# Kernel tuning notes

Measured on AMD Instinct MI355X. Metric: run time of the kernel, lower is better.

Reference implementation:

```python
import jax, jax.numpy as jnp
import numpy as np

N = 20000      # nodes
E = 320000     # edges
H = 256        # hidden_dim
BD = 64        # bond embedding dim
MSG_IN = 2 * H + BD  # 576


def setup_inputs() -> dict:
    key = jax.random.key(0)
    ks = jax.random.split(key, 24)
    s = 0.05
    inp = {}
    inp["x"] = jax.random.randint(ks[0], (N, 3), 0, 7).astype(jnp.float32)
    inp["edge_index"] = jax.random.randint(ks[1], (2, E), 0, N).astype(jnp.int32)
    inp["edge_attr"] = jax.random.randint(ks[2], (E, 1), 0, 5).astype(jnp.float32)
    inp["batch"] = jnp.zeros((N,), jnp.int32)
    # embedding tables
    inp["atom_table"] = jax.random.normal(ks[3], (11, 64), jnp.float32) * s
    inp["charge_table"] = jax.random.normal(ks[4], (7, 32), jnp.float32) * s
    inp["hybrid_table"] = jax.random.normal(ks[5], (8, 32), jnp.float32) * s
    inp["bond_table"] = jax.random.normal(ks[6], (5, BD), jnp.float32) * s
    # 3 stacked ChemicalGraphConv layers (weights stored [in, out])
    inp["gnn_w1"] = jax.random.normal(ks[7], (3, MSG_IN, H), jnp.float32) * s
    inp["gnn_b1"] = jnp.zeros((3, H), jnp.float32)
    inp["gnn_w2"] = jax.random.normal(ks[8], (3, H, H), jnp.float32) * s
    inp["gnn_b2"] = jnp.zeros((3, H), jnp.float32)
    inp["att_w"] = jax.random.normal(ks[9], (3, BD, 1), jnp.float32) * s
    inp["att_b"] = jnp.zeros((3, 1), jnp.float32)
    # chemical_properties MLP
    inp["prop_w1"] = jax.random.normal(ks[10], (H, 128), jnp.float32) * s
    inp["prop_b1"] = jnp.zeros((128,), jnp.float32)
    inp["prop_w2"] = jax.random.normal(ks[11], (128, 32), jnp.float32) * s
    inp["prop_b2"] = jnp.zeros((32,), jnp.float32)
    # 4 functional-group pattern encoders, stacked [4, H, 16]
    inp["fg_w"] = jax.random.normal(ks[12], (4, H, 16), jnp.float32) * s
    inp["fg_b"] = jnp.zeros((4, 16), jnp.float32)
    return inp


def reference(x, edge_index, edge_attr, batch,
              atom_table, charge_table, hybrid_table, bond_table,
              gnn_w1, gnn_b1, gnn_w2, gnn_b2, att_w, att_b,
              prop_w1, prop_b1, prop_w2, prop_b2, fg_w, fg_b):
    n = x.shape[0]
    atom_types = jnp.clip(x[:, 0].astype(jnp.int32), 0, 10)
    formal_charges = jnp.clip(x[:, 2].astype(jnp.int32) + 3, 0, 6)
    hybridization = jnp.clip(x[:, 1].astype(jnp.int32), 0, 7)
    bond_types = jnp.clip(edge_attr[:, 0].astype(jnp.int32), 0, 4)
    bond_emb = bond_table[bond_types]  # [E, 64]

    h = jnp.concatenate([atom_table[atom_types],
                         charge_table[formal_charges],
                         hybrid_table[hybridization]], axis=-1)  # [N, 128]
    h = jnp.pad(h, ((0, 0), (0, H - h.shape[1])))  # pad to hidden_dim

    row, col = edge_index[0], edge_index[1]
    for l in range(3):  # 3 ChemicalGraphConv layers
        gate = jax.nn.sigmoid(bond_emb @ att_w[l] + att_b[l])            # [E, 1]
        msg = jnp.concatenate([h[row], h[col], bond_emb], axis=-1)      # [E, 576]
        msg = jax.nn.relu(msg @ gnn_w1[l] + gnn_b1[l]) @ gnn_w2[l] + gnn_b2[l]
        msg = msg * gate                                                 # [E, H]
        h = h + jax.ops.segment_sum(msg, row, num_segments=n)

    chemical_props = jax.nn.relu(h @ prop_w1 + prop_b1) @ prop_w2 + prop_b2  # [N, 32]

    # FunctionalGroupDetector: mean(encoder(h)) == mean(h) @ W + b (linear)
    pooled = jnp.mean(h, axis=0)                                   # [H]
    fg = (jnp.einsum('d,kdo->ko', pooled, fg_w) + fg_b).reshape(-1)  # [64]
    fg_features = jnp.broadcast_to(fg, (n, 64))

    return h, chemical_props, fg_features, atom_types
```

## Files before the change

### kernel.cpp

```cpp
#include <hip/hip_runtime.h>
#include <stdint.h>

typedef unsigned short u16;
typedef unsigned int   u32;
typedef unsigned long long u64;
typedef __attribute__((ext_vector_type(8))) short bf16x8;
typedef __attribute__((ext_vector_type(4))) float f32x4;

#define NN 20000
#define NE 320000
#define HD 256
#define BD 64

#define WS_PRE   0u
#define WS_W1T   20480000u
#define WS_W2I   21266432u
#define WS_PW1   21659648u
#define WS_PREB  21725184u
#define WS_GATE  21740544u
#define WS_POOL  21740608u
#define WS_FGV   21741632u
#define WS_CNT   21741888u
#define WS_META  21821888u

__device__ __forceinline__ u16 f2bf(float f){
  u32 u = __float_as_uint(f);
  u += 0x7fffu + ((u >> 16) & 1u);
  return (u16)(u >> 16);
}
__device__ __forceinline__ u32 pk2(float a, float b){
  return (u32)f2bf(a) | ((u32)f2bf(b) << 16);
}
__device__ __forceinline__ float bf2f(u16 u){
  return __uint_as_float((u32)u << 16);
}
__device__ __forceinline__ u32 pk2t(float a, float b){
  return __builtin_amdgcn_perm(__float_as_uint(a), __float_as_uint(b), 0x03020706u);
}
__device__ __forceinline__ u32 relu_pack(u32 a, u32 b, float p0, float p1){
  float a0 = __uint_as_float(a << 16);
  float a1 = __uint_as_float(a & 0xffff0000u);
  float b0 = __uint_as_float(b << 16);
  float b1 = __uint_as_float(b & 0xffff0000u);
  float s0 = fmaxf(a0 + b0 + p0, 0.f);
  float s1 = fmaxf(a1 + b1 + p1, 0.f);
  return pk2t(s0, s1);
}
__device__ __forceinline__ void gl_lds16(const u16* g, u16* l){
  __builtin_amdgcn_global_load_lds(
      (const __attribute__((address_space(1))) unsigned int*)g,
      (__attribute__((address_space(3))) unsigned int*)l, 16, 0, 0);
}

__global__ void setup_k(const float* __restrict__ gw1,
                        const float* __restrict__ gw2,
                        const float* __restrict__ pw1,
                        const float* __restrict__ bond_table,
                        const float* __restrict__ gb1,
                        const float* __restrict__ att_w,
                        const float* __restrict__ att_b,
                        const float* __restrict__ x,
                        const float* __restrict__ atom_table,
                        const float* __restrict__ charge_table,
                        const float* __restrict__ hybrid_table,
                        u16* __restrict__ w1t, u16* __restrict__ w2img,
                        u16* __restrict__ pw1bf, float* __restrict__ preb,
                        float* __restrict__ gate_tab, float* __restrict__ pooled,
                        int* __restrict__ cnt,
                        float* __restrict__ h0, float* __restrict__ out_at){
  int i = blockIdx.x*256 + threadIdx.x;
  if (i < 442368){
    float v = gw1[i];
    int l = i / 147456;
    int r = i - l*147456;
    int srow = r >> 8, c = r & 255;
    if (srow < 512){
      int dc = (srow < 256) ? c : (256 + c);
      w1t[((size_t)l*512 + dc)*256 + (srow & 255)] = f2bf(v);
    }
  } else if (i < 638976){
    int t = i - 442368;
    float v = gw2[t];
    int l = t >> 16;
    int rest = t & 65535;
    int k = rest >> 8, c = rest & 255;
    int ks = k >> 5, k5 = k & 31;
    int kc = k5 >> 3, j = k5 & 7;
    int s = kc ^ ((c >> 1) & 3);
    w2img[(((l*8 + ks)*256 + c)*4 + s)*8 + j] = f2bf(v);
  } else if (i < 671744){
    int t = i - 638976;
    float v = pw1[t];
    int k = t >> 7, o = t & 127;
    pw1bf[o*256 + k] = f2bf(v);
  } else if (i < 675584){
    int t = i - 671744;
    int l = t / 1280;
    int r = t - l*1280;
    int bt = r >> 8, c = r & 255;
    float s = gb1[l*HD + c];
    for (int d = 0; d < BD; ++d)
      s += bond_table[bt*BD + d] * gw1[(l*576 + 512 + d)*256 + c];
    preb[(l*5 + bt)*256 + c] = s;
  } else if (i < 675599){
    int t = i - 675584;
    int l = t / 5, b = t - 5*l;
    float s = att_b[l];
    for (int d = 0; d < BD; ++d) s += bond_table[b*BD + d] * att_w[l*BD + d];
    gate_tab[t] = 1.0f / (1.0f + __expf(-s));
  } else if (i < 675855){
    pooled[i - 675599] = 0.0f;
  } else if (i < 695855){
    cnt[i - 675855] = 0;
  } else if (i < 1335855){
    int t = i - 695855;
    int n = t >> 5, sub = t & 31, c0 = sub*8;
    int at = (int)x[n*3 + 0]; at = at < 0 ? 0 : (at > 10 ? 10 : at);
    float4 v0 = {0.f,0.f,0.f,0.f}, v1 = {0.f,0.f,0.f,0.f};
    if (c0 < 64){
      v0 = *(const float4*)(atom_table + at*64 + c0);
      v1 = *(const float4*)(atom_table + at*64 + c0 + 4);
    } else if (c0 < 96){
      int fc = (int)x[n*3 + 2] + 3; fc = fc < 0 ? 0 : (fc > 6 ? 6 : fc);
      v0 = *(const float4*)(charge_table + fc*32 + (c0 - 64));
      v1 = *(const float4*)(charge_table + fc*32 + (c0 - 64) + 4);
    } else if (c0 < 128){
      int hy = (int)x[n*3 + 1]; hy = hy < 0 ? 0 : (hy > 7 ? 7 : hy);
      v0 = *(const float4*)(hybrid_table + hy*32 + (c0 - 96));
      v1 = *(const float4*)(hybrid_table + hy*32 + (c0 - 96) + 4);
    }
    *(float4*)(h0 + (size_t)n*HD + c0)     = v0;
    *(float4*)(h0 + (size_t)n*HD + c0 + 4) = v1;
    if (sub == 0) out_at[n] = (float)at;
  }
}

__global__ void hist_k(const int* __restrict__ eidx, int* __restrict__ cnt){
  int e = blockIdx.x*256 + threadIdx.x;
  int r = eidx[e]; r = r < 0 ? 0 : (r >= NN ? NN-1 : r);
  atomicAdd(&cnt[r], 1);
}

__launch_bounds__(1024)
__global__ void scan_k(int* __restrict__ cnt){
  __shared__ int part[1024];
  int t = threadIdx.x;
  int base = t*20;
  int loc[20];
  int s = 0;
  #pragma unroll
  for (int j = 0; j < 20; ++j){
    int idx = base + j;
    int v = (idx < NN) ? cnt[idx] : 0;
    loc[j] = v; s += v;
  }
  part[t] = s; __syncthreads();
  for (int off = 1; off < 1024; off <<= 1){
    int v = (t >= off) ? part[t-off] : 0;
    __syncthreads();
    part[t] += v;
    __syncthreads();
  }
  int run = part[t] - s;
  #pragma unroll
  for (int j = 0; j < 20; ++j){
    int idx = base + j;
    if (idx < NN){ cnt[idx] = run; run += loc[j]; }
  }
}

__global__ void scatter_k(const int* __restrict__ eidx,
                          const float* __restrict__ eattr,
                          int* __restrict__ cur,
                          int2* __restrict__ smeta){
  int e = blockIdx.x*256 + threadIdx.x;
  int r = eidx[e];        r = r < 0 ? 0 : (r >= NN ? NN-1 : r);
  int c = eidx[NE + e];   c = c < 0 ? 0 : (c >= NN ? NN-1 : c);
  int bt = (int)eattr[e]; bt = bt < 0 ? 0 : (bt > 4 ? 4 : bt);
  int pos = atomicAdd(&cur[r], 1);
  if (pos >= 0 && pos < NE){
    int2 m; m.x = r | (bt << 20); m.y = c;
    smeta[pos] = m;
  }
}

__launch_bounds__(256, 4)
__global__ void pre_k(const float* __restrict__ h,
                      const u16* __restrict__ w1t,
                      u16* __restrict__ pre, int layer){
  __shared__ u16 a_lds[64*40];
  __shared__ u16 b_lds[256*40];
  const int tid = threadIdx.x;
  const int n0 = blockIdx.x * 64;
  const int half = blockIdx.y;
  const int w = tid >> 6, lane = tid & 63, g = lane >> 4, lr = lane & 15;
  const int rstage = tid >> 2, q = tid & 3;
  int arow = n0 + rstage; if (arow >= NN) arow = NN-1;
  const float* hrow = h + (size_t)arow*HD;
  const u16* bp = w1t + ((size_t)layer*512 + (size_t)half*256 + tid)*256;

  f32x4 acc[4][4];
  for (int mi = 0; mi < 4; ++mi)
    for (int nj = 0; nj < 4; ++nj)
      acc[mi][nj] = (f32x4){0.f,0.f,0.f,0.f};

  for (int ks = 0; ks < 8; ++ks){
    __syncthreads();
    {
      const float* src = hrow + ks*32 + q*8;
      float4 f0 = *(const float4*)src;
      float4 f1 = *(const float4*)(src + 4);
      uint4 av;
      av.x = pk2(f0.x,f0.y); av.y = pk2(f0.z,f0.w);
      av.z = pk2(f1.x,f1.y); av.w = pk2(f1.z,f1.w);
      *(uint4*)(a_lds + rstage*40 + q*8) = av;
    }
    {
      const u16* src = bp + ks*32;
      uint4 s0 = *(const uint4*)(src);
      uint4 s1 = *(const uint4*)(src + 8);
      uint4 s2 = *(const uint4*)(src + 16);
      uint4 s3 = *(const uint4*)(src + 24);
      u16* dst = b_lds + tid*40;
      *(uint4*)(dst)      = s0;
      *(uint4*)(dst + 8)  = s1;
      *(uint4*)(dst + 16) = s2;
      *(uint4*)(dst + 24) = s3;
    }
    __syncthreads();
    bf16x8 af[4], bfr[4];
    for (int mi = 0; mi < 4; ++mi)
      af[mi] = *(const bf16x8*)(a_lds + (mi*16 + lr)*40 + g*8);
    for (int nj = 0; nj < 4; ++nj)
      bfr[nj] = *(const bf16x8*)(b_lds + (w*64 + nj*16 + lr)*40 + g*8);
    for (int mi = 0; mi < 4; ++mi)
      for (int nj = 0; nj < 4; ++nj)
        acc[mi][nj] = __builtin_amdgcn_mfma_f32_16x16x32_bf16(af[mi], bfr[nj], acc[mi][nj], 0, 0, 0);
  }

  for (int mi = 0; mi < 4; ++mi)
    for (int nj = 0; nj < 4; ++nj)
      for (int p = 0; p < 4; ++p){
        int re = mi*16 + g*4 + p;
        int n = n0 + re;
        if (n < NN)
          pre[(size_t)n*512 + half*256 + w*64 + nj*16 + lr] = f2bf(acc[mi][nj][p]);
      }
}

__launch_bounds__(512, 4)
__global__ void edge_msg_k(const int2* __restrict__ smeta,
                           const u16* __restrict__ pre,
                           const float* __restrict__ prebg,
                           const u16* __restrict__ w2img,
                           const float* __restrict__ b2g,
                           const float* __restrict__ gate_tab,
                           float* __restrict__ h,
                           int layer){
  __shared__ u16 b_lds[16384];
  __shared__ u16 t_lds[64*264];
  __shared__ int   row_l[64];
  __shared__ float gate_l[64];
  __shared__ u64   mask_l;

  const int tid = threadIdx.x;
  const int bid = blockIdx.x;
  const int blk = (bid & 7)*625 + (bid >> 3);
  const int eBase = blk * 64;
  const int w = tid >> 6, lane = tid & 63, g = lane >> 4, lr = lane & 15;
  const int rstage = tid >> 3, q = tid & 7;

  const size_t wbase = (size_t)layer*65536;

  #pragma unroll
  for (int b = 0; b < 2; ++b)
    #pragma unroll
    for (int j = 0; j < 2; ++j)
      gl_lds16(w2img + wbase + (size_t)(b*256 + w*32 + j*16)*32 + lane*8,
               b_lds + b*8192 + w*1024 + j*512);

  int2 m0 = smeta[eBase + rstage];
  const int rI  = m0.x & 0xFFFFF;
  const int btI = (m0.x >> 20) & 7;
  const int cI  = m0.y;

  if (tid < 64){
    int2 mm = smeta[eBase + tid];
    int r = mm.x & 0xFFFFF;
    row_l[tid]  = r;
    gate_l[tid] = gate_tab[layer*5 + ((mm.x >> 20) & 7)];
    int rprev = __shfl_up(r, 1);
    bool fl = (tid > 0) && (r != rprev);
    u64 mk = __ballot(fl);
    if (tid == 0) mask_l = mk;
  }

  {
    const u16* p1 = pre + (size_t)rI*512;
    const u16* p2 = pre + (size_t)cI*512 + 256;
    const float* pb = prebg + (size_t)(layer*5 + btI)*256;
    uint4 v1[4], v2[4];
    #pragma unroll
    for (int it = 0; it < 4; ++it){
      int c0 = it*64 + q*8;
      v1[it] = *(const uint4*)(p1 + c0);
      v2[it] = *(const uint4*)(p2 + c0);
    }
    #pragma unroll
    for (int it = 0; it < 4; ++it){
      int c0 = it*64 + q*8;
      float4 pa = *(const float4*)(pb + c0);
      float4 pc = *(const float4*)(pb + c0 + 4);
      uint4 ov;
      ov.x = relu_pack(v1[it].x, v2[it].x, pa.x, pa.y);
      ov.y = relu_pack(v1[it].y, v2[it].y, pa.z, pa.w);
      ov.z = relu_pack(v1[it].z, v2[it].z, pc.x, pc.y);
      ov.w = relu_pack(v1[it].w, v2[it].w, pc.z, pc.w);
      *(uint4*)(t_lds + rstage*264 + c0) = ov;
    }
  }

  __syncthreads();

  f32x4 acc[4][2];
  for (int mi = 0; mi < 4; ++mi)
    for (int nj = 0; nj < 2; ++nj)
      acc[mi][nj] = (f32x4){0.f,0.f,0.f,0.f};

  const int sw = (g ^ ((lr >> 1) & 3)) << 3;

  #pragma unroll
  for (int ks = 0; ks < 8; ++ks){
    if (ks >= 1 && ks < 7){
      #pragma unroll
      for (int j = 0; j < 2; ++j)
        gl_lds16(w2img + wbase + (size_t)((ks+1)*256 + w*32 + j*16)*32 + lane*8,
                 b_lds + ((ks+1)&1)*8192 + w*1024 + j*512);
      asm volatile("s_waitcnt vmcnt(2)" ::: "memory");
    } else if (ks == 0){
      asm volatile("s_waitcnt vmcnt(2)" ::: "memory");
    } else {
      asm volatile("s_waitcnt vmcnt(0)" ::: "memory");
    }
    const u16* bb = b_lds + (ks&1)*8192 + w*1024;
    bf16x8 af[4], bfr[2];
    for (int nj = 0; nj < 2; ++nj)
      bfr[nj] = *(const bf16x8*)(bb + (nj*16 + lr)*32 + sw);
    for (int mi = 0; mi < 4; ++mi)
      af[mi] = *(const bf16x8*)(t_lds + (mi*16 + lr)*264 + ks*32 + g*8);
    __builtin_amdgcn_s_setprio(1);
    for (int mi = 0; mi < 4; ++mi)
      for (int nj = 0; nj < 2; ++nj)
        acc[mi][nj] = __builtin_amdgcn_mfma_f32_16x16x32_bf16(af[mi], bfr[nj], acc[mi][nj], 0, 0, 0);
    __builtin_amdgcn_s_setprio(0);
  }

  {
    float b2v[2];
    for (int nj = 0; nj < 2; ++nj) b2v[nj] = b2g[layer*HD + w*32 + nj*16 + lr];
    for (int mi = 0; mi < 4; ++mi)
      for (int nj = 0; nj < 2; ++nj){
        u16* mb = b_lds + nj*8192 + w*1024 + lr*64;
        float v[4];
        #pragma unroll
        for (int p = 0; p < 4; ++p){
          int re = mi*16 + g*4 + p;
          v[p] = (acc[mi][nj][p] + b2v[nj]) * gate_l[re];
        }
        int slot = (mi*2 + (g >> 1)) ^ (lr & 7);
        uint2 pkv; pkv.x = pk2t(v[0], v[1]); pkv.y = pk2t(v[2], v[3]);
        *(uint2*)(mb + slot*8 + (g & 1)*4) = pkv;
      }
  }
  __syncthreads();

  {
    const int cl = tid & 255, half = tid >> 8;
    u64 mk = mask_l;
    u32 m32 = (u32)(mk >> (half ? 32 : 0));
    m32 = __builtin_amdgcn_readfirstlane(m32);
    const u16* mb = b_lds + ((cl >> 4) & 1)*8192 + (cl >> 5)*1024 + (cl & 15)*64;
    float run = 0.f;
    #pragma unroll
    for (int e8l = 0; e8l < 4; ++e8l){
      int e8 = half*4 + e8l;
      bf16x8 mv = *(const bf16x8*)(mb + ((e8 ^ (cl & 7)) << 3));
      #pragma unroll
      for (int j = 0; j < 8; ++j){
        int el = e8l*8 + j;
        run += bf2f((u16)mv[j]);
        bool fl = (el == 31) || ((m32 >> (el + 1)) & 1u);
        if (fl){
          int rr = row_l[half*32 + el];
          atomicAdd(h + (size_t)rr*HD + cl, run);
          run = 0.f;
        }
      }
    }
  }
}

__global__ void pool_k(const float* __restrict__ h,
                       float* __restrict__ pooled){
  int c = threadIdx.x;
  int r0 = blockIdx.x * 50;
  float s = 0.f;
  for (int r = r0; r < r0 + 50; ++r)
    s += h[(size_t)r*HD + c];
  atomicAdd(&pooled[c], s);
}

__global__ void fg_k(const float* __restrict__ pooled,
                     const float* __restrict__ fg_w,
                     const float* __restrict__ fg_b,
                     float* __restrict__ fg_vals){
  int o = threadIdx.x;
  int k = o >> 4, j = o & 15;
  float s = 0.f;
  for (int d = 0; d < HD; ++d) s += pooled[d] * fg_w[(size_t)k*HD*16 + d*16 + j];
  fg_vals[o] = s / (float)NN + fg_b[k*16 + j];
}

__global__ void bcast_fg_k(const float* __restrict__ fg_vals,
                           float* __restrict__ out_fg){
  __shared__ float fv[64];
  if (threadIdx.x < 64) fv[threadIdx.x] = fg_vals[threadIdx.x];
  __syncthreads();
  int i = blockIdx.x*256 + threadIdx.x;
  out_fg[i] = fv[i & 63];
}

__launch_bounds__(256, 3)
__global__ void props_mfma_k(const float* __restrict__ h,
                             const u16* __restrict__ pw1bf,
                             const float* __restrict__ pb1,
                             const float* __restrict__ pw2,
                             const float* __restrict__ pb2,
                             float* __restrict__ outp){
  __shared__ u16 a_lds[64*40];
  __shared__ u16 b2_lds[128*40];
  __shared__ u16 t2[64*136];
  __shared__ float w2s[128*32];
  const int tid = threadIdx.x;
  const int n0 = blockIdx.x*64;
  const int w = tid >> 6, lane = tid & 63, g = lane >> 4, lr = lane & 15;
  const int rstage = tid >> 2, q = tid & 3;
  int arow = n0 + rstage; if (arow >= NN) arow = NN-1;
  const float* hrow = h + (size_t)arow*HD;

  for (int j = 0; j < 4; ++j)
    *(float4*)(w2s + tid*16 + j*4) = *(const float4*)(pw2 + tid*16 + j*4);

  const int colb = tid >> 1, halfb = tid & 1;

  f32x4 acc[4][2];
  for (int mi = 0; mi < 4; ++mi)
    for (int nj = 0; nj < 2; ++nj)
      acc[mi][nj] = (f32x4){0.f,0.f,0.f,0.f};

  for (int ks = 0; ks < 8; ++ks){
    __syncthreads();
    {
      const float* src = hrow + ks*32 + q*8;
      float4 f0 = *(const float4*)src;
      float4 f1 = *(const float4*)(src + 4);
      uint4 av;
      av.x = pk2(f0.x,f0.y); av.y = pk2(f0.z,f0.w);
      av.z = pk2(f1.x,f1.y); av.w = pk2(f1.z,f1.w);
      *(uint4*)(a_lds + rstage*40 + q*8) = av;
    }
    {
      const u16* src = pw1bf + colb*256 + ks*32 + halfb*16;
      uint4 s0 = *(const uint4*)src;
      uint4 s1 = *(const uint4*)(src + 8);
      u16* dst = b2_lds + colb*40 + halfb*16;
      *(uint4*)dst = s0; *(uint4*)(dst + 8) = s1;
    }
    __syncthreads();
    bf16x8 af[4], bfr[2];
    for (int mi = 0; mi < 4; ++mi)
      af[mi] = *(const bf16x8*)(a_lds + (mi*16 + lr)*40 + g*8);
    for (int nj = 0; nj < 2; ++nj)
      bfr[nj] = *(const bf16x8*)(b2_lds + (w*32 + nj*16 + lr)*40 + g*8);
    for (int mi = 0; mi < 4; ++mi)
      for (int nj = 0; nj < 2; ++nj)
        acc[mi][nj] = __builtin_amdgcn_mfma_f32_16x16x32_bf16(af[mi], bfr[nj], acc[mi][nj], 0, 0, 0);
  }

  {
    float b1v[2];
    for (int nj = 0; nj < 2; ++nj) b1v[nj] = pb1[w*32 + nj*16 + lr];
    for (int mi = 0; mi < 4; ++mi)
      for (int nj = 0; nj < 2; ++nj){
        int colt = w*32 + nj*16 + lr;
        for (int p = 0; p < 4; ++p){
          float v = acc[mi][nj][p] + b1v[nj];
          v = v > 0.f ? v : 0.f;
          t2[(mi*16 + g*4 + p)*136 + colt] = f2bf(v);
        }
      }
  }
  __syncthreads();

  {
    int e = tid >> 2, o0 = (tid & 3)*8;
    int n = n0 + e;
    float ap[8];
    #pragma unroll
    for (int o = 0; o < 8; ++o) ap[o] = pb2[o0 + o];
    for (int d0 = 0; d0 < 16; ++d0){
      bf16x8 tv = *(const bf16x8*)(t2 + e*136 + d0*8);
      #pragma unroll
      for (int dd = 0; dd < 8; ++dd){
        float t = bf2f((u16)tv[dd]);
        const float* wr = w2s + (d0*8 + dd)*32 + o0;
        #pragma unroll
        for (int o = 0; o < 8; ++o) ap[o] += t * wr[o];
      }
    }
    if (n < NN){
      *(float4*)(outp + (size_t)n*32 + o0)     = *(float4*)(ap);
      *(float4*)(outp + (size_t)n*32 + o0 + 4) = *(float4*)(ap + 4);
    }
  }
}

extern "C" void kernel_launch(void* const* d_in, const int* in_sizes, int n_in,
                              void* d_out, int out_size, void* d_ws, size_t ws_size,
                              hipStream_t stream) {
  const float* x            = (const float*)d_in[0];
  const int*   eidx         = (const int*)  d_in[1];
  const float* eattr        = (const float*)d_in[2];
  const float* atom_table   = (const float*)d_in[4];
  const float* charge_table = (const float*)d_in[5];
  const float* hybrid_table = (const float*)d_in[6];
  const float* bond_table   = (const float*)d_in[7];
  const float* gw1          = (const float*)d_in[8];
  const float* gb1          = (const float*)d_in[9];
  const float* gw2          = (const float*)d_in[10];
  const float* gb2          = (const float*)d_in[11];
  const float* attw         = (const float*)d_in[12];
  const float* attb         = (const float*)d_in[13];
  const float* pw1          = (const float*)d_in[14];
  const float* pb1          = (const float*)d_in[15];
  const float* pw2          = (const float*)d_in[16];
  const float* pb2          = (const float*)d_in[17];
  const float* fgw          = (const float*)d_in[18];
  const float* fgb          = (const float*)d_in[19];

  float* out       = (float*)d_out;
  float* out_h     = out;
  float* out_props = out + (size_t)NN*HD;
  float* out_fg    = out_props + (size_t)NN*32;
  float* out_at    = out_fg + (size_t)NN*64;

  char* ws = (char*)d_ws;
  u16*   pre      = (u16*)  (ws + WS_PRE);
  u16*   w1t      = (u16*)  (ws + WS_W1T);
  u16*   w2img    = (u16*)  (ws + WS_W2I);
  u16*   pw1bf    = (u16*)  (ws + WS_PW1);
  float* prebg    = (float*)(ws + WS_PREB);
  float* gate_tab = (float*)(ws + WS_GATE);
  float* pooled   = (float*)(ws + WS_POOL);
  float* fg_vals  = (float*)(ws + WS_FGV);
  int*   cnt      = (int*)  (ws + WS_CNT);
  int2*  smeta    = (int2*) (ws + WS_META);

  setup_k<<<5219, 256, 0, stream>>>(gw1, gw2, pw1, bond_table, gb1, attw, attb,
                                    x, atom_table, charge_table, hybrid_table,
                                    w1t, w2img, pw1bf, prebg, gate_tab, pooled,
                                    cnt, out_h, out_at);

  hist_k<<<1250, 256, 0, stream>>>(eidx, cnt);
  scan_k<<<1, 1024, 0, stream>>>(cnt);
  scatter_k<<<1250, 256, 0, stream>>>(eidx, eattr, cnt, smeta);

  for (int l = 0; l < 3; ++l){
    pre_k<<<dim3(313, 2), 256, 0, stream>>>(out_h, w1t, pre, l);
    edge_msg_k<<<5000, 512, 0, stream>>>(smeta, pre, prebg, w2img,
                                         gb2, gate_tab, out_h, l);
  }

  pool_k<<<400, 256, 0, stream>>>(out_h, pooled);
  fg_k<<<1, 64, 0, stream>>>(pooled, fgw, fgb, fg_vals);
  props_mfma_k<<<313, 256, 0, stream>>>(out_h, pw1bf, pb1, pw2, pb2, out_props);
  bcast_fg_k<<<5000, 256, 0, stream>>>(fg_vals, out_fg);
}
```

Before: 382.9 us.

## Merge pre_k halves per block, hoist b2 bias into segment sums, MFMA props layer 2

pre_k now computes all 512 output columns per block, so each block converts and loads the h tile once instead of twice, at the cost of more accumulators and lower occupancy. edge_msg_k drops the per-element b2 bias add. Instead it adds b2 times the prefix-summed gate difference once per segment flush. The props second layer moves from scalar FMA to bf16 MFMA using a bf16 copy of pw2 prepared in setup, which adds bf16 rounding to that GEMM.

```diff
diff --git a/kernel.cpp b/kernel.cpp
--- a/kernel.cpp
+++ b/kernel.cpp
@@ -16,12 +16,13 @@
 #define WS_W1T   20480000u
 #define WS_W2I   21266432u
 #define WS_PW1   21659648u
-#define WS_PREB  21725184u
-#define WS_GATE  21740544u
-#define WS_POOL  21740608u
-#define WS_FGV   21741632u
-#define WS_CNT   21741888u
-#define WS_META  21821888u
+#define WS_PW2   21725184u
+#define WS_PREB  21733376u
+#define WS_GATE  21748736u
+#define WS_POOL  21748800u
+#define WS_FGV   21749824u
+#define WS_CNT   21750080u
+#define WS_META  21830080u
 
 __device__ __forceinline__ u16 f2bf(float f){
   u32 u = __float_as_uint(f);
@@ -55,6 +56,7 @@
 __global__ void setup_k(const float* __restrict__ gw1,
                         const float* __restrict__ gw2,
                         const float* __restrict__ pw1,
+                        const float* __restrict__ pw2,
                         const float* __restrict__ bond_table,
                         const float* __restrict__ gb1,
                         const float* __restrict__ att_w,
@@ -64,7 +66,8 @@
                         const float* __restrict__ charge_table,
                         const float* __restrict__ hybrid_table,
                         u16* __restrict__ w1t, u16* __restrict__ w2img,
-                        u16* __restrict__ pw1bf, float* __restrict__ preb,
+                        u16* __restrict__ pw1bf, u16* __restrict__ pw2bf,
+                        float* __restrict__ preb,
                         float* __restrict__ gate_tab, float* __restrict__ pooled,
                         int* __restrict__ cnt,
                         float* __restrict__ h0, float* __restrict__ out_at){
@@ -93,8 +96,13 @@
     float v = pw1[t];
     int k = t >> 7, o = t & 127;
     pw1bf[o*256 + k] = f2bf(v);
-  } else if (i < 675584){
+  } else if (i < 675840){
     int t = i - 671744;
+    float v = pw2[t];
+    int k = t >> 5, o = t & 31;
+    pw2bf[o*128 + k] = f2bf(v);
+  } else if (i < 679680){
+    int t = i - 675840;
     int l = t / 1280;
     int r = t - l*1280;
     int bt = r >> 8, c = r & 255;
@@ -102,18 +110,18 @@
     for (int d = 0; d < BD; ++d)
       s += bond_table[bt*BD + d] * gw1[(l*576 + 512 + d)*256 + c];
     preb[(l*5 + bt)*256 + c] = s;
-  } else if (i < 675599){
-    int t = i - 675584;
+  } else if (i < 679695){
+    int t = i - 679680;
     int l = t / 5, b = t - 5*l;
     float s = att_b[l];
     for (int d = 0; d < BD; ++d) s += bond_table[b*BD + d] * att_w[l*BD + d];
     gate_tab[t] = 1.0f / (1.0f + __expf(-s));
-  } else if (i < 675855){
-    pooled[i - 675599] = 0.0f;
-  } else if (i < 695855){
-    cnt[i - 675855] = 0;
-  } else if (i < 1335855){
-    int t = i - 695855;
+  } else if (i < 679951){
+    pooled[i - 679695] = 0.0f;
+  } else if (i < 699951){
+    cnt[i - 679951] = 0;
+  } else if (i < 1339951){
+    int t = i - 699951;
     int n = t >> 5, sub = t & 31, c0 = sub*8;
     int at = (int)x[n*3 + 0]; at = at < 0 ? 0 : (at > 10 ? 10 : at);
     float4 v0 = {0.f,0.f,0.f,0.f}, v1 = {0.f,0.f,0.f,0.f};
@@ -184,24 +192,25 @@
   }
 }
 
-__launch_bounds__(256, 4)
+__launch_bounds__(256, 2)
 __global__ void pre_k(const float* __restrict__ h,
                       const u16* __restrict__ w1t,
                       u16* __restrict__ pre, int layer){
   __shared__ u16 a_lds[64*40];
-  __shared__ u16 b_lds[256*40];
+  __shared__ u16 b_lds[512*40];
   const int tid = threadIdx.x;
   const int n0 = blockIdx.x * 64;
-  const int half = blockIdx.y;
   const int w = tid >> 6, lane = tid & 63, g = lane >> 4, lr = lane & 15;
   const int rstage = tid >> 2, q = tid & 3;
   int arow = n0 + rstage; if (arow >= NN) arow = NN-1;
   const float* hrow = h + (size_t)arow*HD;
-  const u16* bp = w1t + ((size_t)layer*512 + (size_t)half*256 + tid)*256;
-
-  f32x4 acc[4][4];
+  const u16* bp0 = w1t + ((size_t)layer*512 + tid)*256;
+  const u16* bp1 = bp0 + 256*256;
+
+  f32x4 acc[4][8];
   for (int mi = 0; mi < 4; ++mi)
-    for (int nj = 0; nj < 4; ++nj)
+    #pragma unroll
+    for (int nj = 0; nj < 8; ++nj)
       acc[mi][nj] = (f32x4){0.f,0.f,0.f,0.f};
 
   for (int ks = 0; ks < 8; ++ks){
@@ -216,35 +225,49 @@
       *(uint4*)(a_lds + rstage*40 + q*8) = av;
     }
     {
-      const u16* src = bp + ks*32;
-      uint4 s0 = *(const uint4*)(src);
-      uint4 s1 = *(const uint4*)(src + 8);
-      uint4 s2 = *(const uint4*)(src + 16);
-      uint4 s3 = *(const uint4*)(src + 24);
+      const u16* s0p = bp0 + ks*32;
+      const u16* s1p = bp1 + ks*32;
+      uint4 s0 = *(const uint4*)(s0p);
+      uint4 s1 = *(const uint4*)(s0p + 8);
+      uint4 s2 = *(const uint4*)(s0p + 16);
+      uint4 s3 = *(const uint4*)(s0p + 24);
       u16* dst = b_lds + tid*40;
       *(uint4*)(dst)      = s0;
       *(uint4*)(dst + 8)  = s1;
       *(uint4*)(dst + 16) = s2;
       *(uint4*)(dst + 24) = s3;
+      uint4 t0 = *(const uint4*)(s1p);
+      uint4 t1 = *(const uint4*)(s1p + 8);
+      uint4 t2v = *(const uint4*)(s1p + 16);
+      uint4 t3 = *(const uint4*)(s1p + 24);
+      u16* dst1 = b_lds + (tid + 256)*40;
+      *(uint4*)(dst1)      = t0;
+      *(uint4*)(dst1 + 8)  = t1;
+      *(uint4*)(dst1 + 16) = t2v;
+      *(uint4*)(dst1 + 24) = t3;
     }
     __syncthreads();
-    bf16x8 af[4], bfr[4];
+    bf16x8 af[4], bfr[8];
     for (int mi = 0; mi < 4; ++mi)
       af[mi] = *(const bf16x8*)(a_lds + (mi*16 + lr)*40 + g*8);
-    for (int nj = 0; nj < 4; ++nj)
-      bfr[nj] = *(const bf16x8*)(b_lds + (w*64 + nj*16 + lr)*40 + g*8);
-    for (int mi = 0; mi < 4; ++mi)
-      for (int nj = 0; nj < 4; ++nj)
+    #pragma unroll
+    for (int nj = 0; nj < 8; ++nj)
+      bfr[nj] = *(const bf16x8*)(b_lds + (w*128 + nj*16 + lr)*40 + g*8);
+    for (int mi = 0; mi < 4; ++mi)
+      #pragma unroll
+      for (int nj = 0; nj < 8; ++nj)
         acc[mi][nj] = __builtin_amdgcn_mfma_f32_16x16x32_bf16(af[mi], bfr[nj], acc[mi][nj], 0, 0, 0);
   }
 
   for (int mi = 0; mi < 4; ++mi)
-    for (int nj = 0; nj < 4; ++nj)
+    #pragma unroll
+    for (int nj = 0; nj < 8; ++nj)
       for (int p = 0; p < 4; ++p){
         int re = mi*16 + g*4 + p;
         int n = n0 + re;
+        int col = w*128 + nj*16 + lr;
         if (n < NN)
-          pre[(size_t)n*512 + half*256 + w*64 + nj*16 + lr] = f2bf(acc[mi][nj][p]);
+          pre[(size_t)n*512 + col] = f2bf(acc[mi][nj][p]);
       }
 }
 
@@ -261,6 +284,7 @@
   __shared__ u16 t_lds[64*264];
   __shared__ int   row_l[64];
   __shared__ float gate_l[64];
+  __shared__ float gps_l[64];
   __shared__ u64   mask_l;
 
   const int tid = threadIdx.x;
@@ -287,8 +311,16 @@
   if (tid < 64){
     int2 mm = smeta[eBase + tid];
     int r = mm.x & 0xFFFFF;
-    row_l[tid]  = r;
-    gate_l[tid] = gate_tab[layer*5 + ((mm.x >> 20) & 7)];
+    row_l[tid] = r;
+    float gt = gate_tab[layer*5 + ((mm.x >> 20) & 7)];
+    gate_l[tid] = gt;
+    float ps = gt;
+    #pragma unroll
+    for (int off = 1; off < 64; off <<= 1){
+      float o = __shfl_up(ps, off);
+      if (tid >= off) ps += o;
+    }
+    gps_l[tid] = ps;
     int rprev = __shfl_up(r, 1);
     bool fl = (tid > 0) && (r != rprev);
     u64 mk = __ballot(fl);
@@ -356,8 +388,6 @@
   }
 
   {
-    float b2v[2];
-    for (int nj = 0; nj < 2; ++nj) b2v[nj] = b2g[layer*HD + w*32 + nj*16 + lr];
     for (int mi = 0; mi < 4; ++mi)
       for (int nj = 0; nj < 2; ++nj){
         u16* mb = b_lds + nj*8192 + w*1024 + lr*64;
@@ -365,7 +395,7 @@
         #pragma unroll
         for (int p = 0; p < 4; ++p){
           int re = mi*16 + g*4 + p;
-          v[p] = (acc[mi][nj][p] + b2v[nj]) * gate_l[re];
+          v[p] = acc[mi][nj][p] * gate_l[re];
         }
         int slot = (mi*2 + (g >> 1)) ^ (lr & 7);
         uint2 pkv; pkv.x = pk2t(v[0], v[1]); pkv.y = pk2t(v[2], v[3]);
@@ -376,11 +406,13 @@
 
   {
     const int cl = tid & 255, half = tid >> 8;
+    float b2v = b2g[layer*HD + cl];
     u64 mk = mask_l;
     u32 m32 = (u32)(mk >> (half ? 32 : 0));
     m32 = __builtin_amdgcn_readfirstlane(m32);
     const u16* mb = b_lds + ((cl >> 4) & 1)*8192 + (cl >> 5)*1024 + (cl & 15)*64;
     float run = 0.f;
+    float gprev = half ? gps_l[31] : 0.f;
     #pragma unroll
     for (int e8l = 0; e8l < 4; ++e8l){
       int e8 = half*4 + e8l;
@@ -391,8 +423,11 @@
         run += bf2f((u16)mv[j]);
         bool fl = (el == 31) || ((m32 >> (el + 1)) & 1u);
         if (fl){
-          int rr = row_l[half*32 + el];
-          atomicAdd(h + (size_t)rr*HD + cl, run);
+          int ae = half*32 + el;
+          float gc = gps_l[ae];
+          int rr = row_l[ae];
+          atomicAdd(h + (size_t)rr*HD + cl, fmaf(b2v, gc - gprev, run));
+          gprev = gc;
           run = 0.f;
         }
       }
@@ -434,22 +469,18 @@
 __global__ void props_mfma_k(const float* __restrict__ h,
                              const u16* __restrict__ pw1bf,
                              const float* __restrict__ pb1,
-                             const float* __restrict__ pw2,
+                             const u16* __restrict__ pw2bf,
                              const float* __restrict__ pb2,
                              float* __restrict__ outp){
   __shared__ u16 a_lds[64*40];
   __shared__ u16 b2_lds[128*40];
   __shared__ u16 t2[64*136];
-  __shared__ float w2s[128*32];
   const int tid = threadIdx.x;
   const int n0 = blockIdx.x*64;
   const int w = tid >> 6, lane = tid & 63, g = lane >> 4, lr = lane & 15;
   const int rstage = tid >> 2, q = tid & 3;
   int arow = n0 + rstage; if (arow >= NN) arow = NN-1;
   const float* hrow = h + (size_t)arow*HD;
-
-  for (int j = 0; j < 4; ++j)
-    *(float4*)(w2s + tid*16 + j*4) = *(const float4*)(pw2 + tid*16 + j*4);
 
   const int colb = tid >> 1, halfb = tid & 1;
 
@@ -503,25 +534,31 @@
   __syncthreads();
 
   {
-    int e = tid >> 2, o0 = (tid & 3)*8;
-    int n = n0 + e;
-    float ap[8];
-    #pragma unroll
-    for (int o = 0; o < 8; ++o) ap[o] = pb2[o0 + o];
-    for (int d0 = 0; d0 < 16; ++d0){
-      bf16x8 tv = *(const bf16x8*)(t2 + e*136 + d0*8);
-      #pragma unroll
-      for (int dd = 0; dd < 8; ++dd){
-        float t = bf2f((u16)tv[dd]);
-        const float* wr = w2s + (d0*8 + dd)*32 + o0;
-        #pragma unroll
-        for (int o = 0; o < 8; ++o) ap[o] += t * wr[o];
+    int col = tid >> 3, part = tid & 7;
+    const u16* src = pw2bf + col*128 + part*16;
+    u16* dst = b2_lds + col*136 + part*16;
+    *(uint4*)dst       = *(const uint4*)src;
+    *(uint4*)(dst + 8) = *(const uint4*)(src + 8);
+  }
+  __syncthreads();
+
+  {
+    f32x4 acc2[2];
+    for (int nj = 0; nj < 2; ++nj) acc2[nj] = (f32x4){0.f,0.f,0.f,0.f};
+    for (int ks = 0; ks < 4; ++ks){
+      bf16x8 af = *(const bf16x8*)(t2 + (w*16 + lr)*136 + ks*32 + g*8);
+      for (int nj = 0; nj < 2; ++nj){
+        bf16x8 bf = *(const bf16x8*)(b2_lds + (nj*16 + lr)*136 + ks*32 + g*8);
+        acc2[nj] = __builtin_amdgcn_mfma_f32_16x16x32_bf16(af, bf, acc2[nj], 0, 0, 0);
       }
     }
-    if (n < NN){
-      *(float4*)(outp + (size_t)n*32 + o0)     = *(float4*)(ap);
-      *(float4*)(outp + (size_t)n*32 + o0 + 4) = *(float4*)(ap + 4);
-    }
+    for (int nj = 0; nj < 2; ++nj)
+      for (int p = 0; p < 4; ++p){
+        int n = n0 + w*16 + g*4 + p;
+        int col = nj*16 + lr;
+        if (n < NN)
+          outp[(size_t)n*32 + col] = acc2[nj][p] + pb2[col];
+      }
   }
 }
 
@@ -559,6 +596,7 @@
   u16*   w1t      = (u16*)  (ws + WS_W1T);
   u16*   w2img    = (u16*)  (ws + WS_W2I);
   u16*   pw1bf    = (u16*)  (ws + WS_PW1);
+  u16*   pw2bf    = (u16*)  (ws + WS_PW2);
   float* prebg    = (float*)(ws + WS_PREB);
   float* gate_tab = (float*)(ws + WS_GATE);
   float* pooled   = (float*)(ws + WS_POOL);
@@ -566,9 +604,9 @@
   int*   cnt      = (int*)  (ws + WS_CNT);
   int2*  smeta    = (int2*) (ws + WS_META);
 
-  setup_k<<<5219, 256, 0, stream>>>(gw1, gw2, pw1, bond_table, gb1, attw, attb,
+  setup_k<<<5235, 256, 0, stream>>>(gw1, gw2, pw1, pw2, bond_table, gb1, attw, attb,
                                     x, atom_table, charge_table, hybrid_table,
-                                    w1t, w2img, pw1bf, prebg, gate_tab, pooled,
+                                    w1t, w2img, pw1bf, pw2bf, prebg, gate_tab, pooled,
                                     cnt, out_h, out_at);
 
   hist_k<<<1250, 256, 0, stream>>>(eidx, cnt);
@@ -576,13 +614,13 @@
   scatter_k<<<1250, 256, 0, stream>>>(eidx, eattr, cnt, smeta);
 
   for (int l = 0; l < 3; ++l){
-    pre_k<<<dim3(313, 2), 256, 0, stream>>>(out_h, w1t, pre, l);
+    pre_k<<<313, 256, 0, stream>>>(out_h, w1t, pre, l);
     edge_msg_k<<<5000, 512, 0, stream>>>(smeta, pre, prebg, w2img,
                                          gb2, gate_tab, out_h, l);
   }
 
   pool_k<<<400, 256, 0, stream>>>(out_h, pooled);
   fg_k<<<1, 64, 0, stream>>>(pooled, fgw, fgb, fg_vals);
-  props_mfma_k<<<313, 256, 0, stream>>>(out_h, pw1bf, pb1, pw2, pb2, out_props);
+  props_mfma_k<<<313, 256, 0, stream>>>(out_h, pw1bf, pb1, pw2bf, pb2, out_props);
   bcast_fg_k<<<5000, 256, 0, stream>>>(fg_vals, out_fg);
 }
```

Result: slower. 392.1 us (+2.4%).
